# Performance work log

Measured on AMD Instinct MI355X. Metric: run time of the kernel, lower is better.

The kernel has to match this reference:

```python
import jax, jax.numpy as jnp
import numpy as np

DIM = 384
HD = 64
SCALE = float(HD ** 0.5)


def _linear_params(key, out_f, in_f):
    kw, kb = jax.random.split(key)
    bound = 1.0 / np.sqrt(in_f)
    W = jax.random.uniform(kw, (out_f, in_f), jnp.float32, -bound, bound)
    b = jax.random.uniform(kb, (out_f,), jnp.float32, -bound, bound)
    return W, b


def setup_inputs() -> dict:
    key = jax.random.key(0)
    ks = jax.random.split(key, 12)
    N = 8192
    situation = jax.random.normal(ks[0], (DIM,), jnp.float32)
    turn_embeddings = jax.random.normal(ks[1], (N, DIM), jnp.float32)
    bilinear_scores = jax.random.normal(ks[2], (N,), jnp.float32)
    Wt, bt = _linear_params(ks[3], HD, DIM + 1)      # turn_proj
    Ws, bs = _linear_params(ks[4], HD, DIM)          # situation_proj
    Wsaq, bsaq = _linear_params(ks[5], HD, HD)
    Wsak, bsak = _linear_params(ks[6], HD, HD)
    Wsav, bsav = _linear_params(ks[7], HD, HD)
    Wcq, bcq = _linear_params(ks[8], HD, HD)
    Wck, bck = _linear_params(ks[9], HD, HD)
    Wcv, bcv = _linear_params(ks[10], HD, HD)
    # score_head is zero-initialized in the module; use small random values so
    # the output is non-trivial for kernel correctness testing.
    Wsc, bsc = _linear_params(ks[11], 1, HD)
    residual_gate = jnp.float32(-5.0)
    return dict(situation=situation, turn_embeddings=turn_embeddings,
                bilinear_scores=bilinear_scores,
                Wt=Wt, bt=bt, Ws=Ws, bs=bs,
                Wsaq=Wsaq, bsaq=bsaq, Wsak=Wsak, bsak=bsak, Wsav=Wsav, bsav=bsav,
                Wcq=Wcq, bcq=bcq, Wck=Wck, bck=bck, Wcv=Wcv, bcv=bcv,
                Wsc=Wsc, bsc=bsc, residual_gate=residual_gate)


def reference(situation, turn_embeddings, bilinear_scores,
              Wt, bt, Ws, bs,
              Wsaq, bsaq, Wsak, bsak, Wsav, bsav,
              Wcq, bcq, Wck, bck, Wcv, bcv,
              Wsc, bsc, residual_gate):
    # [N, dim+1] = [turn_embedding; bilinear_score]
    turn_features = jnp.concatenate([turn_embeddings, bilinear_scores[:, None]], axis=-1)
    turn_hidden = turn_features @ Wt.T + bt                      # [N, HD]
    # self-attention among turns (dropout = identity, eval mode)
    sa_q = turn_hidden @ Wsaq.T + bsaq
    sa_k = turn_hidden @ Wsak.T + bsak
    sa_v = turn_hidden @ Wsav.T + bsav
    sa_weights = jax.nn.softmax((sa_q @ sa_k.T) / SCALE, axis=-1)  # [N, N]
    turn_hidden = turn_hidden + sa_weights @ sa_v
    # sigmoid cross-attention against the single situation vector
    sit_hidden = (situation @ Ws.T + bs)[None, :]                # [1, HD]
    ca_q = turn_hidden @ Wcq.T + bcq                             # [N, HD]
    ca_k = sit_hidden @ Wck.T + bck                              # [1, HD]
    ca_v = sit_hidden @ Wcv.T + bcv                              # [1, HD]
    ca_weights = jax.nn.sigmoid((ca_q @ ca_k.T) / SCALE)         # [N, 1]
    combined = turn_hidden + ca_weights * ca_v                   # [N, HD]
    attention_scores = (combined @ Wsc.T + bsc)[:, 0]            # [N]
    gate = jax.nn.sigmoid(residual_gate)
    return (1.0 - gate) * bilinear_scores + gate * attention_scores
```

## Files before the change

kernel.cpp:

```cpp
#include <hip/hip_runtime.h>
#include <hip/hip_bf16.h>

typedef __attribute__((ext_vector_type(8))) short short8;
typedef __attribute__((ext_vector_type(4))) float f32x4;
typedef __attribute__((ext_vector_type(2))) long long2t;

__device__ __forceinline__ short f2bf(float x) {
  union { float f; unsigned u; } a; a.f = x;
  unsigned r = (a.u + 0x7FFFu + ((a.u >> 16) & 1u)) >> 16;
  return (short)r;
}
__device__ __forceinline__ float bf2f(short x) {
  union { unsigned u; float f; } a; a.u = ((unsigned)(unsigned short)x) << 16;
  return a.f;
}
__device__ __forceinline__ unsigned cvtpk(float lo, float hi) {
  unsigned r;
  asm("v_cvt_pk_bf16_f32 %0, %1, %2" : "=v"(r) : "v"(lo), "v"(hi));
  return r;
}
__device__ __forceinline__ unsigned pk8(float a, float b, float c, float d) {
  unsigned lo, hi;
  asm("v_cvt_pk_fp8_f32 %0, %1, %2" : "=v"(lo) : "v"(a), "v"(b));
  asm("v_cvt_pk_fp8_f32 %0, %1, %2" : "=v"(hi) : "v"(c), "v"(d));
  return (lo & 0xffffu) | (hi << 16);
}
__device__ __forceinline__ long2t as_l2(uint4 v) {
  union { uint4 u; long2t l; } cc; cc.u = v; return cc.l;
}
__device__ __forceinline__ void gload16(const void* g, void* l) {
  __builtin_amdgcn_global_load_lds((const __attribute__((address_space(1))) unsigned int*)g,
                                   (__attribute__((address_space(3))) unsigned int*)l, 16, 0, 0);
}

__global__ __launch_bounds__(256) void ca_proj4(
    const float* __restrict__ te, const float* __restrict__ bil,
    const float* __restrict__ Wt, const float* __restrict__ bt,
    const float* __restrict__ Wsaq, const float* __restrict__ bq,
    const float* __restrict__ Wsak, const float* __restrict__ bk2,
    const float* __restrict__ Wsav, const float* __restrict__ bv,
    short* __restrict__ hb, unsigned char* __restrict__ qb8,
    unsigned char* __restrict__ kb8, unsigned char* __restrict__ vl8,
    const float* __restrict__ sit, const float* __restrict__ Ws, const float* __restrict__ bs,
    const float* __restrict__ Wck, const float* __restrict__ bck,
    const float* __restrict__ Wcv, const float* __restrict__ bcv,
    const float* __restrict__ Wcq, const float* __restrict__ bcq,
    const float* __restrict__ Wsc, float* __restrict__ u_ws, float* __restrict__ scal,
    int N) {
  __shared__ float Pp[8192];
  __shared__ short Hl[32][72];
  __shared__ unsigned char Q8[32][72];
  __shared__ unsigned char K8[32][72];
  __shared__ unsigned char V8s[64][32];
  __shared__ float part[4][64];
  __shared__ float sh[64], ck[64], cv[64];
  const int t = threadIdx.x;
  if ((int)blockIdx.x == (N >> 5)) {
    int j = t & 63, p = t >> 6;
    float a = 0.f;
    for (int d = p * 96; d < p * 96 + 96; ++d) a += Ws[j * 384 + d] * sit[d];
    part[p][j] = a;
    __syncthreads();
    if (t < 64) sh[t] = part[0][t] + part[1][t] + part[2][t] + part[3][t] + bs[t];
    __syncthreads();
    if (t < 64) {
      float kk = bck[t], vv = bcv[t];
      for (int d = 0; d < 64; ++d) { kk += Wck[t * 64 + d] * sh[d]; vv += Wcv[t * 64 + d] * sh[d]; }
      ck[t] = kk; cv[t] = vv;
    }
    __syncthreads();
    if (t < 64) {
      float uu = 0.f;
      for (int jj = 0; jj < 64; ++jj) uu += Wcq[jj * 64 + t] * ck[jj];
      u_ws[t] = uu;
    }
    if (t == 0) {
      float c0 = 0.f, cw = 0.f;
      for (int jj = 0; jj < 64; ++jj) { c0 += bcq[jj] * ck[jj]; cw += cv[jj] * Wsc[jj]; }
      scal[0] = c0; scal[1] = cw;
    }
    return;
  }
  const int lane = t & 63, w = t >> 6;
  const int g = lane >> 4, li = lane & 15;
  const int i0 = blockIdx.x * 32;

  f32x4 acc[2][4];
#pragma unroll
  for (int qs = 0; qs < 2; ++qs)
#pragma unroll
    for (int n = 0; n < 4; ++n) acc[qs][n] = (f32x4){0.f, 0.f, 0.f, 0.f};
  const int kw = w * 96;
#pragma unroll
  for (int ks = 0; ks < 3; ++ks) {
    short8 af[2];
#pragma unroll
    for (int qs = 0; qs < 2; ++qs) {
      const float* ap = te + (size_t)(i0 + qs * 16 + li) * 384 + kw + ks * 32 + g * 8;
      float4 a0 = *(const float4*)ap;
      float4 a1 = *(const float4*)(ap + 4);
      af[qs][0] = f2bf(a0.x); af[qs][1] = f2bf(a0.y); af[qs][2] = f2bf(a0.z); af[qs][3] = f2bf(a0.w);
      af[qs][4] = f2bf(a1.x); af[qs][5] = f2bf(a1.y); af[qs][6] = f2bf(a1.z); af[qs][7] = f2bf(a1.w);
    }
#pragma unroll
    for (int n = 0; n < 4; ++n) {
      short8 bf;
      const float* wp = Wt + (size_t)(n * 16 + li) * 385 + kw + ks * 32 + g * 8;
#pragma unroll
      for (int jj = 0; jj < 8; ++jj) bf[jj] = f2bf(wp[jj]);
      acc[0][n] = __builtin_amdgcn_mfma_f32_16x16x32_bf16(af[0], bf, acc[0][n], 0, 0, 0);
      acc[1][n] = __builtin_amdgcn_mfma_f32_16x16x32_bf16(af[1], bf, acc[1][n], 0, 0, 0);
    }
  }
#pragma unroll
  for (int qs = 0; qs < 2; ++qs)
#pragma unroll
    for (int n = 0; n < 4; ++n)
      *(f32x4*)&Pp[((w * 8 + qs * 4 + n) * 64 + lane) * 4] = acc[qs][n];
  __syncthreads();
#pragma unroll
  for (int ss = 0; ss < 2; ++ss) {
    int s = t + ss * 256;
    int qs2 = s >> 8, n2 = (s >> 6) & 3, lane2 = s & 63;
    int g2 = lane2 >> 4, li2 = lane2 & 15;
    int base = (qs2 * 4 + n2) * 256 + lane2 * 4;
    f32x4 v0 = *(const f32x4*)&Pp[base];
    f32x4 v1 = *(const f32x4*)&Pp[base + 2048];
    f32x4 v2 = *(const f32x4*)&Pp[base + 4096];
    f32x4 v3 = *(const f32x4*)&Pp[base + 6144];
    int col = n2 * 16 + li2;
    float wc = Wt[(size_t)col * 385 + 384], bb = bt[col];
#pragma unroll
    for (int r = 0; r < 4; ++r) {
      int row = qs2 * 16 + g2 * 4 + r;
      float val = v0[r] + v1[r] + v2[r] + v3[r] + bb + bil[i0 + row] * wc;
      Hl[row][col] = f2bf(val);
    }
  }
  __syncthreads();
  {
    int row = t >> 3, seg = t & 7;
    *(uint4*)&hb[(size_t)(i0 + row) * 64 + seg * 8] = *(uint4*)&Hl[row][seg * 8];
  }
  short8 ha[2][2];
#pragma unroll
  for (int qs = 0; qs < 2; ++qs)
#pragma unroll
    for (int ks = 0; ks < 2; ++ks)
      ha[qs][ks] = *(const short8*)&Hl[qs * 16 + li][ks * 32 + g * 8];
  const float* Wm[3] = {Wsaq, Wsak, Wsav};
  f32x4 pacc[3][2];
#pragma unroll
  for (int m = 0; m < 3; ++m)
#pragma unroll
    for (int qs = 0; qs < 2; ++qs) pacc[m][qs] = (f32x4){0.f, 0.f, 0.f, 0.f};
#pragma unroll
  for (int m = 0; m < 3; ++m)
#pragma unroll
    for (int ks = 0; ks < 2; ++ks) {
      const float* wp = Wm[m] + (size_t)(w * 16 + li) * 64 + ks * 32 + g * 8;
      float4 b0 = *(const float4*)wp;
      float4 b1 = *(const float4*)(wp + 4);
      short8 bf;
      bf[0] = f2bf(b0.x); bf[1] = f2bf(b0.y); bf[2] = f2bf(b0.z); bf[3] = f2bf(b0.w);
      bf[4] = f2bf(b1.x); bf[5] = f2bf(b1.y); bf[6] = f2bf(b1.z); bf[7] = f2bf(b1.w);
      pacc[m][0] = __builtin_amdgcn_mfma_f32_16x16x32_bf16(ha[0][ks], bf, pacc[m][0], 0, 0, 0);
      pacc[m][1] = __builtin_amdgcn_mfma_f32_16x16x32_bf16(ha[1][ks], bf, pacc[m][1], 0, 0, 0);
    }
  const int col = w * 16 + li;
  const float QSC = 0.18033688011112042f;
  {
    float bbq = bq[col], bbk = bk2[col], bbv = bv[col];
#pragma unroll
    for (int qs = 0; qs < 2; ++qs) {
      unsigned uq = pk8((pacc[0][qs][0] + bbq) * QSC, (pacc[0][qs][1] + bbq) * QSC,
                        (pacc[0][qs][2] + bbq) * QSC, (pacc[0][qs][3] + bbq) * QSC);
      unsigned uk = pk8(pacc[1][qs][0] + bbk, pacc[1][qs][1] + bbk,
                        pacc[1][qs][2] + bbk, pacc[1][qs][3] + bbk);
      unsigned uv = pk8(pacc[2][qs][0] + bbv, pacc[2][qs][1] + bbv,
                        pacc[2][qs][2] + bbv, pacc[2][qs][3] + bbv);
#pragma unroll
      for (int r = 0; r < 4; ++r) {
        Q8[qs * 16 + g * 4 + r][col] = (unsigned char)(uq >> (8 * r));
        K8[qs * 16 + g * 4 + r][col] = (unsigned char)(uk >> (8 * r));
      }
      *(unsigned*)&V8s[col][qs * 16 + g * 4] = uv;
    }
  }
  __syncthreads();
  {
    const int h = t & 1, l2 = (t >> 1) & 63, loc = t >> 7;
    const int srow = (l2 & 15) + 16 * loc;
    const int scol = h * 32 + (l2 >> 4) * 8;
    unsigned long vq = *(const unsigned long*)&Q8[srow][scol];
    *(unsigned long*)(qb8 + ((size_t)((i0 >> 4) + loc) * 1024 + l2 * 16 + h * 8)) = vq;
    unsigned long vk = *(const unsigned long*)&K8[srow][scol];
    *(unsigned long*)(kb8 + ((size_t)((i0 >> 6) * 4 + ((i0 >> 4) & 3) + loc) * 1024 + l2 * 16 + h * 8)) = vk;
    const int dt = t >> 6, l3 = t & 63;
    unsigned long vv = *(const unsigned long*)&V8s[dt * 16 + (l3 & 15)][(l3 >> 4) * 8];
    *(unsigned long*)(vl8 + ((size_t)((i0 >> 6) * 4 + dt) * 1024 + l3 * 16 + ((i0 >> 5) & 1) * 8)) = vv;
  }
}

__global__ __launch_bounds__(128, 2) void ca_attn7(
    const uint4* __restrict__ qb8, const unsigned* __restrict__ kb8,
    const unsigned* __restrict__ vl8,
    unsigned* __restrict__ pOu, float* __restrict__ pL, int N) {
  __shared__ unsigned Kl[2][1024];
  __shared__ unsigned Vl[2][1024];
  __shared__ unsigned Pl[2][2][256];
  const int t = threadIdx.x, lane = t & 63, wid = t >> 6;
  const int g = lane >> 4, li = lane & 15;
  const int bid = blockIdx.x;
  const int sp = bid & 7, qblk = bid >> 3;
  const int i0 = qblk * 64 + wid * 32;
  const int ntil = N >> 9;
  const int tile0 = sp * ntil;

#define STG(b, T)                                                                       \
  do {                                                                                  \
    gload16(kb8 + (((size_t)(T) * 4 + 2 * wid) << 8) + lane * 4,     &Kl[b][(2 * wid) * 256]);     \
    gload16(kb8 + (((size_t)(T) * 4 + 2 * wid + 1) << 8) + lane * 4, &Kl[b][(2 * wid + 1) * 256]); \
    gload16(vl8 + (((size_t)(T) * 4 + 2 * wid) << 8) + lane * 4,     &Vl[b][(2 * wid) * 256]);     \
    gload16(vl8 + (((size_t)(T) * 4 + 2 * wid + 1) << 8) + lane * 4, &Vl[b][(2 * wid + 1) * 256]); \
  } while (0)

  long2t qf[2];
  qf[0] = as_l2(qb8[(size_t)((i0 >> 4) + 0) * 64 + lane]);
  qf[1] = as_l2(qb8[(size_t)((i0 >> 4) + 1) * 64 + lane]);

  f32x4 acc[2][4];
  float rs[2] = {0.f, 0.f};
#pragma unroll
  for (int qs = 0; qs < 2; ++qs)
#pragma unroll
    for (int n = 0; n < 4; ++n) acc[qs][n] = (f32x4){0.f, 0.f, 0.f, 0.f};

  STG(0, tile0);
  asm volatile("s_waitcnt vmcnt(0)" ::: "memory");

  for (int tt = 0; tt < ntil; ++tt) {
    const int cur = tt & 1;
    __builtin_amdgcn_s_barrier();
    if (tt + 1 < ntil) STG(cur ^ 1, tile0 + tt + 1);

    f32x4 s4[2][4];
#pragma unroll
    for (int qs = 0; qs < 2; ++qs)
#pragma unroll
      for (int t4 = 0; t4 < 4; ++t4) s4[qs][t4] = (f32x4){0.f, 0.f, 0.f, 0.f};
    __builtin_amdgcn_s_setprio(1);
#pragma unroll
    for (int t4 = 0; t4 < 4; ++t4) {
      long2t kl = as_l2(*(const uint4*)&Kl[cur][t4 * 256 + lane * 4]);
      s4[0][t4] = __builtin_amdgcn_mfma_f32_16x16x32_fp8_fp8(kl.x, qf[0].x, s4[0][t4], 0, 0, 0);
      s4[0][t4] = __builtin_amdgcn_mfma_f32_16x16x32_fp8_fp8(kl.y, qf[0].y, s4[0][t4], 0, 0, 0);
      s4[1][t4] = __builtin_amdgcn_mfma_f32_16x16x32_fp8_fp8(kl.x, qf[1].x, s4[1][t4], 0, 0, 0);
      s4[1][t4] = __builtin_amdgcn_mfma_f32_16x16x32_fp8_fp8(kl.y, qf[1].y, s4[1][t4], 0, 0, 0);
    }
    __builtin_amdgcn_s_setprio(0);
#pragma unroll
    for (int qs = 0; qs < 2; ++qs) {
#pragma unroll
      for (int t4 = 0; t4 < 4; ++t4) {
        float p0, p1, p2, p3;
        asm("v_exp_f32 %0, %1" : "=v"(p0) : "v"(s4[qs][t4][0]));
        asm("v_exp_f32 %0, %1" : "=v"(p1) : "v"(s4[qs][t4][1]));
        asm("v_exp_f32 %0, %1" : "=v"(p2) : "v"(s4[qs][t4][2]));
        asm("v_exp_f32 %0, %1" : "=v"(p3) : "v"(s4[qs][t4][3]));
        rs[qs] += (p0 + p1) + (p2 + p3);
        unsigned u = pk8(p0, p1, p2, p3);
        Pl[wid][qs][(li + 16 * ((t4 & 1) * 2 + (g >> 1))) * 4 + (t4 >> 1) * 2 + (g & 1)] = u;
      }
    }
    asm volatile("s_waitcnt lgkmcnt(0)" ::: "memory");
#pragma unroll
    for (int qs = 0; qs < 2; ++qs) {
      long2t pf = as_l2(*(const uint4*)&Pl[wid][qs][lane * 4]);
      __builtin_amdgcn_s_setprio(1);
#pragma unroll
      for (int dt = 0; dt < 4; ++dt) {
        long2t vf = as_l2(*(const uint4*)&Vl[cur][dt * 256 + lane * 4]);
        acc[qs][dt] = __builtin_amdgcn_mfma_f32_16x16x32_fp8_fp8(pf.x, vf.x, acc[qs][dt], 0, 0, 0);
        acc[qs][dt] = __builtin_amdgcn_mfma_f32_16x16x32_fp8_fp8(pf.y, vf.y, acc[qs][dt], 0, 0, 0);
      }
      __builtin_amdgcn_s_setprio(0);
    }
    asm volatile("s_waitcnt vmcnt(0)" ::: "memory");
  }
#undef STG

  const size_t ob = ((size_t)sp * (N >> 5) + (i0 >> 5)) * 2;
#pragma unroll
  for (int qs = 0; qs < 2; ++qs) {
#pragma unroll
    for (int dt = 0; dt < 4; ++dt) {
      uint2 wv;
      wv.x = cvtpk(acc[qs][dt][0], acc[qs][dt][1]);
      wv.y = cvtpk(acc[qs][dt][2], acc[qs][dt][3]);
      *(uint2*)&pOu[((ob + qs) * 4 + dt) * 128 + lane * 2] = wv;
    }
    float r2 = rs[qs] + __shfl_xor(rs[qs], 16, 64);
    r2 += __shfl_xor(r2, 32, 64);
    if (lane < 16) pL[(size_t)sp * N + i0 + qs * 16 + lane] = r2;
  }
}

__global__ __launch_bounds__(256) void ca_merge3(
    const short* __restrict__ hb, const unsigned* __restrict__ pOu, const float* __restrict__ pL,
    const float* __restrict__ u_ws, const float* __restrict__ scal,
    const float* __restrict__ bil, const float* __restrict__ Wsc,
    const float* __restrict__ bsc_p, const float* __restrict__ rgate_p,
    float* __restrict__ out, int N) {
  const int t = threadIdx.x;
  const int rp = t >> 3, e = t & 7;
  const int dt2 = e >> 1, li0 = (e & 1) * 8;
  const float gate = 1.f / (1.f + __expf(-rgate_p[0]));
  const float bsc = bsc_p[0], sc0 = scal[0], sc1 = scal[1];
  const int R0 = blockIdx.x * 64 + rp * 2;
  const int b32 = R0 >> 5, qs2 = (R0 >> 4) & 1, g2 = (R0 >> 2) & 3;
  const int rpair = (R0 & 3) >> 1;
  float o0[8], o1[8], L0 = 0.f, L1 = 0.f;
#pragma unroll
  for (int j = 0; j < 8; ++j) { o0[j] = 0.f; o1[j] = 0.f; }
#pragma unroll
  for (int sp2 = 0; sp2 < 8; ++sp2) {
    size_t base = ((((size_t)sp2 * (N >> 5) + b32) * 2 + qs2) * 4 + dt2) * 128
                  + (g2 * 16 + li0) * 2 + rpair;
#pragma unroll
    for (int j = 0; j < 8; ++j) {
      unsigned u = pOu[base + 2 * j];
      o0[j] += bf2f((short)(u & 0xffff));
      o1[j] += bf2f((short)(u >> 16));
    }
    L0 += pL[(size_t)sp2 * N + R0];
    L1 += pL[(size_t)sp2 * N + R0 + 1];
  }
  const float iL0 = 1.f / L0, iL1 = 1.f / L1;
  const int c0 = dt2 * 16 + li0;
  short8 hv0 = *(const short8*)&hb[(size_t)R0 * 64 + c0];
  short8 hv1 = *(const short8*)&hb[(size_t)(R0 + 1) * 64 + c0];
  float s1a = 0.f, s2a = 0.f, s1b = 0.f, s2b = 0.f;
#pragma unroll
  for (int j = 0; j < 8; ++j) {
    float uwsj = u_ws[c0 + j], wscj = Wsc[c0 + j];
    float h0 = bf2f(hv0[j]) + o0[j] * iL0;
    float h1 = bf2f(hv1[j]) + o1[j] * iL1;
    s1a += h0 * uwsj; s2a += h0 * wscj;
    s1b += h1 * uwsj; s2b += h1 * wscj;
  }
#pragma unroll
  for (int mask = 1; mask < 8; mask <<= 1) {
    s1a += __shfl_xor(s1a, mask, 64);
    s2a += __shfl_xor(s2a, mask, 64);
    s1b += __shfl_xor(s1b, mask, 64);
    s2b += __shfl_xor(s2b, mask, 64);
  }
  if (e == 0) {
    float cawa = 1.f / (1.f + __expf(-(s1a + sc0) * 0.125f));
    float cawb = 1.f / (1.f + __expf(-(s1b + sc0) * 0.125f));
    float scoreA = s2a + cawa * sc1 + bsc;
    float scoreB = s2b + cawb * sc1 + bsc;
    out[R0] = (1.f - gate) * bil[R0] + gate * scoreA;
    out[R0 + 1] = (1.f - gate) * bil[R0 + 1] + gate * scoreB;
  }
}

extern "C" void kernel_launch(void* const* d_in, const int* in_sizes, int n_in,
                              void* d_out, int out_size, void* d_ws, size_t ws_size,
                              hipStream_t stream) {
  const float* sit  = (const float*)d_in[0];
  const float* te   = (const float*)d_in[1];
  const float* bil  = (const float*)d_in[2];
  const float* Wt   = (const float*)d_in[3];
  const float* bt   = (const float*)d_in[4];
  const float* Ws   = (const float*)d_in[5];
  const float* bs   = (const float*)d_in[6];
  const float* Wsaq = (const float*)d_in[7];
  const float* bsaq = (const float*)d_in[8];
  const float* Wsak = (const float*)d_in[9];
  const float* bsak = (const float*)d_in[10];
  const float* Wsav = (const float*)d_in[11];
  const float* bsav = (const float*)d_in[12];
  const float* Wcq  = (const float*)d_in[13];
  const float* bcq  = (const float*)d_in[14];
  const float* Wck  = (const float*)d_in[15];
  const float* bck  = (const float*)d_in[16];
  const float* Wcv  = (const float*)d_in[17];
  const float* bcv  = (const float*)d_in[18];
  const float* Wsc  = (const float*)d_in[19];
  const float* bsc  = (const float*)d_in[20];
  const float* rgate= (const float*)d_in[21];
  const int N = in_sizes[2];

  char* w = (char*)d_ws;
  size_t off = 0;
  short* hbuf        = (short*)(w + off);         off += (size_t)N * 64 * 2;
  unsigned char* qb8 = (unsigned char*)(w + off); off += (size_t)N * 64;
  unsigned char* kb8 = (unsigned char*)(w + off); off += (size_t)N * 64;
  unsigned char* vl8 = (unsigned char*)(w + off); off += (size_t)N * 64;
  float* u_ws        = (float*)(w + off);         off += 64 * 4;
  float* scal        = (float*)(w + off);         off += 4 * 4;
  unsigned* pOu      = (unsigned*)(w + off);      off += (size_t)8 * N * 64 * 2;
  float* pL          = (float*)(w + off);         off += (size_t)8 * N * 4;

  ca_proj4<<<N / 32 + 1, 256, 0, stream>>>(te, bil, Wt, bt, Wsaq, bsaq, Wsak, bsak,
                                           Wsav, bsav, hbuf, qb8, kb8, vl8,
                                           sit, Ws, bs, Wck, bck, Wcv, bcv, Wcq, bcq, Wsc,
                                           u_ws, scal, N);
  ca_attn7<<<N / 8, 128, 0, stream>>>((const uint4*)qb8, (const unsigned*)kb8,
                                      (const unsigned*)vl8, pOu, pL, N);
  ca_merge3<<<N / 64, 256, 0, stream>>>(hbuf, pOu, pL, u_ws, scal, bil, Wsc, bsc, rgate,
                                        (float*)d_out, N);
}
```

Measured before the change: 50.61 us.

## Fold Q/K/V projections into turn projection via precombined weight matrix

Adds a small pre-kernel that multiplies the Q/K/V weights into the turn projection weights (and folds the bilinear column and biases), producing a 256x384 bf16 combined matrix. The projection kernel then does one K=384 GEMM per wave yielding H, Q, K and V directly, removing the cross-wave split-K reduction through shared memory, the second chained GEMM and several block barriers. It also reorders the PV MFMA loop in the attention kernel to share V fragment loads across both query subtiles. This costs an extra kernel launch and four times the MFMA work on the 384-wide input, and it changes rounding because Q/K/V no longer pass through bf16-rounded H.

New measurement: 61.69 us. +21.9%, slower.

```diff
diff --git a/kernel.cpp b/kernel.cpp
--- a/kernel.cpp
+++ b/kernel.cpp
@@ -33,29 +33,50 @@
                                    (__attribute__((address_space(3))) unsigned int*)l, 16, 0, 0);
 }
 
-__global__ __launch_bounds__(256) void ca_proj4(
-    const float* __restrict__ te, const float* __restrict__ bil,
+#define QSC 0.18033688011112042f
+
+__global__ __launch_bounds__(256) void ca_comb(
     const float* __restrict__ Wt, const float* __restrict__ bt,
-    const float* __restrict__ Wsaq, const float* __restrict__ bq,
-    const float* __restrict__ Wsak, const float* __restrict__ bk2,
-    const float* __restrict__ Wsav, const float* __restrict__ bv,
-    short* __restrict__ hb, unsigned char* __restrict__ qb8,
-    unsigned char* __restrict__ kb8, unsigned char* __restrict__ vl8,
+    const float* __restrict__ Wsaq, const float* __restrict__ bsaq,
+    const float* __restrict__ Wsak, const float* __restrict__ bsak,
+    const float* __restrict__ Wsav, const float* __restrict__ bsav,
+    short* __restrict__ Wcomb, float* __restrict__ wcol4, float* __restrict__ bias4,
     const float* __restrict__ sit, const float* __restrict__ Ws, const float* __restrict__ bs,
     const float* __restrict__ Wck, const float* __restrict__ bck,
     const float* __restrict__ Wcv, const float* __restrict__ bcv,
     const float* __restrict__ Wcq, const float* __restrict__ bcq,
-    const float* __restrict__ Wsc, float* __restrict__ u_ws, float* __restrict__ scal,
-    int N) {
-  __shared__ float Pp[8192];
-  __shared__ short Hl[32][72];
-  __shared__ unsigned char Q8[32][72];
-  __shared__ unsigned char K8[32][72];
-  __shared__ unsigned char V8s[64][32];
+    const float* __restrict__ Wsc, float* __restrict__ u_ws, float* __restrict__ scal) {
+  const int bid = blockIdx.x, t = threadIdx.x;
+  if (bid < 96) {
+    __shared__ float Wtc[64][4];
+    const int c0 = bid * 4;
+    { int j = t & 63, cc = t >> 6; Wtc[j][cc] = Wt[(size_t)j * 385 + c0 + cc]; }
+    __syncthreads();
+    const int r = t;
+    float o[4] = {0.f, 0.f, 0.f, 0.f};
+    if (r < 64) {
+#pragma unroll
+      for (int cc = 0; cc < 4; ++cc) o[cc] = Wtc[r][cc];
+    } else {
+      const int m = (r >> 6) - 1, rr = r & 63;
+      const float* Wm = (m == 0 ? Wsaq : m == 1 ? Wsak : Wsav) + (size_t)rr * 64;
+      for (int j = 0; j < 64; ++j) {
+        float wv = Wm[j];
+#pragma unroll
+        for (int cc = 0; cc < 4; ++cc) o[cc] += wv * Wtc[j][cc];
+      }
+      if (m == 0) {
+#pragma unroll
+        for (int cc = 0; cc < 4; ++cc) o[cc] *= QSC;
+      }
+    }
+#pragma unroll
+    for (int cc = 0; cc < 4; ++cc) Wcomb[(size_t)r * 384 + c0 + cc] = f2bf(o[cc]);
+    return;
+  }
   __shared__ float part[4][64];
   __shared__ float sh[64], ck[64], cv[64];
-  const int t = threadIdx.x;
-  if ((int)blockIdx.x == (N >> 5)) {
+  {
     int j = t & 63, p = t >> 6;
     float a = 0.f;
     for (int d = p * 96; d < p * 96 + 96; ++d) a += Ws[j * 384 + d] * sit[d];
@@ -75,13 +96,47 @@
       u_ws[t] = uu;
     }
     if (t == 0) {
-      float c0 = 0.f, cw = 0.f;
-      for (int jj = 0; jj < 64; ++jj) { c0 += bcq[jj] * ck[jj]; cw += cv[jj] * Wsc[jj]; }
-      scal[0] = c0; scal[1] = cw;
-    }
-    return;
-  }
-  const int lane = t & 63, w = t >> 6;
+      float c0s = 0.f, cw = 0.f;
+      for (int jj = 0; jj < 64; ++jj) { c0s += bcq[jj] * ck[jj]; cw += cv[jj] * Wsc[jj]; }
+      scal[0] = c0s; scal[1] = cw;
+    }
+  }
+  {
+    const int r = t;
+    float wc, bb;
+    if (r < 64) {
+      wc = Wt[(size_t)r * 385 + 384];
+      bb = bt[r];
+    } else {
+      const int m = (r >> 6) - 1, rr = r & 63;
+      const float* Wm = (m == 0 ? Wsaq : m == 1 ? Wsak : Wsav) + (size_t)rr * 64;
+      const float* bm = (m == 0 ? bsaq : m == 1 ? bsak : bsav);
+      float s1 = 0.f, s2 = 0.f;
+      for (int j = 0; j < 64; ++j) {
+        float wv = Wm[j];
+        s1 += wv * Wt[(size_t)j * 385 + 384];
+        s2 += wv * bt[j];
+      }
+      float sc = (m == 0) ? QSC : 1.f;
+      wc = sc * s1;
+      bb = sc * (s2 + bm[rr]);
+    }
+    wcol4[r] = wc;
+    bias4[r] = bb;
+  }
+}
+
+__global__ __launch_bounds__(256) void ca_proj5(
+    const float* __restrict__ te, const float* __restrict__ bil,
+    const short* __restrict__ Wcomb, const float* __restrict__ wcol4,
+    const float* __restrict__ bias4,
+    short* __restrict__ hb, unsigned char* __restrict__ qb8,
+    unsigned char* __restrict__ kb8, unsigned char* __restrict__ vl8, int N) {
+  __shared__ short Hl[32][72];
+  __shared__ unsigned char Q8[32][72];
+  __shared__ unsigned char K8[32][72];
+  __shared__ unsigned char V8s[64][32];
+  const int t = threadIdx.x, lane = t & 63, w = t >> 6;
   const int g = lane >> 4, li = lane & 15;
   const int i0 = blockIdx.x * 32;
 
@@ -90,13 +145,13 @@
   for (int qs = 0; qs < 2; ++qs)
 #pragma unroll
     for (int n = 0; n < 4; ++n) acc[qs][n] = (f32x4){0.f, 0.f, 0.f, 0.f};
-  const int kw = w * 96;
-#pragma unroll
-  for (int ks = 0; ks < 3; ++ks) {
+
+#pragma unroll 4
+  for (int ks = 0; ks < 12; ++ks) {
     short8 af[2];
 #pragma unroll
     for (int qs = 0; qs < 2; ++qs) {
-      const float* ap = te + (size_t)(i0 + qs * 16 + li) * 384 + kw + ks * 32 + g * 8;
+      const float* ap = te + (size_t)(i0 + qs * 16 + li) * 384 + ks * 32 + g * 8;
       float4 a0 = *(const float4*)ap;
       float4 a1 = *(const float4*)(ap + 4);
       af[qs][0] = f2bf(a0.x); af[qs][1] = f2bf(a0.y); af[qs][2] = f2bf(a0.z); af[qs][3] = f2bf(a0.w);
@@ -104,101 +159,104 @@
     }
 #pragma unroll
     for (int n = 0; n < 4; ++n) {
-      short8 bf;
-      const float* wp = Wt + (size_t)(n * 16 + li) * 385 + kw + ks * 32 + g * 8;
-#pragma unroll
-      for (int jj = 0; jj < 8; ++jj) bf[jj] = f2bf(wp[jj]);
+      short8 bf = *(const short8*)&Wcomb[(size_t)(w * 64 + n * 16 + li) * 384 + ks * 32 + g * 8];
       acc[0][n] = __builtin_amdgcn_mfma_f32_16x16x32_bf16(af[0], bf, acc[0][n], 0, 0, 0);
       acc[1][n] = __builtin_amdgcn_mfma_f32_16x16x32_bf16(af[1], bf, acc[1][n], 0, 0, 0);
     }
   }
+
+  float bilv[2][4];
 #pragma unroll
   for (int qs = 0; qs < 2; ++qs)
 #pragma unroll
-    for (int n = 0; n < 4; ++n)
-      *(f32x4*)&Pp[((w * 8 + qs * 4 + n) * 64 + lane) * 4] = acc[qs][n];
-  __syncthreads();
-#pragma unroll
-  for (int ss = 0; ss < 2; ++ss) {
-    int s = t + ss * 256;
-    int qs2 = s >> 8, n2 = (s >> 6) & 3, lane2 = s & 63;
-    int g2 = lane2 >> 4, li2 = lane2 & 15;
-    int base = (qs2 * 4 + n2) * 256 + lane2 * 4;
-    f32x4 v0 = *(const f32x4*)&Pp[base];
-    f32x4 v1 = *(const f32x4*)&Pp[base + 2048];
-    f32x4 v2 = *(const f32x4*)&Pp[base + 4096];
-    f32x4 v3 = *(const f32x4*)&Pp[base + 6144];
-    int col = n2 * 16 + li2;
-    float wc = Wt[(size_t)col * 385 + 384], bb = bt[col];
-#pragma unroll
-    for (int r = 0; r < 4; ++r) {
-      int row = qs2 * 16 + g2 * 4 + r;
-      float val = v0[r] + v1[r] + v2[r] + v3[r] + bb + bil[i0 + row] * wc;
-      Hl[row][col] = f2bf(val);
-    }
-  }
-  __syncthreads();
-  {
-    int row = t >> 3, seg = t & 7;
-    *(uint4*)&hb[(size_t)(i0 + row) * 64 + seg * 8] = *(uint4*)&Hl[row][seg * 8];
-  }
-  short8 ha[2][2];
-#pragma unroll
-  for (int qs = 0; qs < 2; ++qs)
-#pragma unroll
-    for (int ks = 0; ks < 2; ++ks)
-      ha[qs][ks] = *(const short8*)&Hl[qs * 16 + li][ks * 32 + g * 8];
-  const float* Wm[3] = {Wsaq, Wsak, Wsav};
-  f32x4 pacc[3][2];
-#pragma unroll
-  for (int m = 0; m < 3; ++m)
-#pragma unroll
-    for (int qs = 0; qs < 2; ++qs) pacc[m][qs] = (f32x4){0.f, 0.f, 0.f, 0.f};
-#pragma unroll
-  for (int m = 0; m < 3; ++m)
-#pragma unroll
-    for (int ks = 0; ks < 2; ++ks) {
-      const float* wp = Wm[m] + (size_t)(w * 16 + li) * 64 + ks * 32 + g * 8;
-      float4 b0 = *(const float4*)wp;
-      float4 b1 = *(const float4*)(wp + 4);
-      short8 bf;
-      bf[0] = f2bf(b0.x); bf[1] = f2bf(b0.y); bf[2] = f2bf(b0.z); bf[3] = f2bf(b0.w);
-      bf[4] = f2bf(b1.x); bf[5] = f2bf(b1.y); bf[6] = f2bf(b1.z); bf[7] = f2bf(b1.w);
-      pacc[m][0] = __builtin_amdgcn_mfma_f32_16x16x32_bf16(ha[0][ks], bf, pacc[m][0], 0, 0, 0);
-      pacc[m][1] = __builtin_amdgcn_mfma_f32_16x16x32_bf16(ha[1][ks], bf, pacc[m][1], 0, 0, 0);
-    }
-  const int col = w * 16 + li;
-  const float QSC = 0.18033688011112042f;
-  {
-    float bbq = bq[col], bbk = bk2[col], bbv = bv[col];
+    for (int r = 0; r < 4; ++r) bilv[qs][r] = bil[i0 + qs * 16 + g * 4 + r];
+  float bb[4], wc[4];
+#pragma unroll
+  for (int n = 0; n < 4; ++n) {
+    bb[n] = bias4[w * 64 + n * 16 + li];
+    wc[n] = wcol4[w * 64 + n * 16 + li];
+  }
+
+  if (w == 0) {
+#pragma unroll
+    for (int qs = 0; qs < 2; ++qs)
+#pragma unroll
+      for (int n = 0; n < 4; ++n)
+#pragma unroll
+        for (int r = 0; r < 4; ++r)
+          Hl[qs * 16 + g * 4 + r][n * 16 + li] =
+              f2bf(acc[qs][n][r] + bb[n] + bilv[qs][r] * wc[n]);
+    asm volatile("s_waitcnt lgkmcnt(0)" ::: "memory");
+    __builtin_amdgcn_sched_barrier(0);
+    const int row = lane >> 1, sb = (lane & 1) * 4;
+#pragma unroll
+    for (int k = 0; k < 4; ++k)
+      *(uint4*)&hb[(size_t)(i0 + row) * 64 + (sb + k) * 8] = *(const uint4*)&Hl[row][(sb + k) * 8];
+  } else if (w == 1) {
+#pragma unroll
+    for (int qs = 0; qs < 2; ++qs)
+#pragma unroll
+      for (int n = 0; n < 4; ++n) {
+        unsigned u = pk8(acc[qs][n][0] + bb[n] + bilv[qs][0] * wc[n],
+                         acc[qs][n][1] + bb[n] + bilv[qs][1] * wc[n],
+                         acc[qs][n][2] + bb[n] + bilv[qs][2] * wc[n],
+                         acc[qs][n][3] + bb[n] + bilv[qs][3] * wc[n]);
+#pragma unroll
+        for (int r = 0; r < 4; ++r)
+          Q8[qs * 16 + g * 4 + r][n * 16 + li] = (unsigned char)(u >> (8 * r));
+      }
+    asm volatile("s_waitcnt lgkmcnt(0)" ::: "memory");
+    __builtin_amdgcn_sched_barrier(0);
 #pragma unroll
     for (int qs = 0; qs < 2; ++qs) {
-      unsigned uq = pk8((pacc[0][qs][0] + bbq) * QSC, (pacc[0][qs][1] + bbq) * QSC,
-                        (pacc[0][qs][2] + bbq) * QSC, (pacc[0][qs][3] + bbq) * QSC);
-      unsigned uk = pk8(pacc[1][qs][0] + bbk, pacc[1][qs][1] + bbk,
-                        pacc[1][qs][2] + bbk, pacc[1][qs][3] + bbk);
-      unsigned uv = pk8(pacc[2][qs][0] + bbv, pacc[2][qs][1] + bbv,
-                        pacc[2][qs][2] + bbv, pacc[2][qs][3] + bbv);
-#pragma unroll
-      for (int r = 0; r < 4; ++r) {
-        Q8[qs * 16 + g * 4 + r][col] = (unsigned char)(uq >> (8 * r));
-        K8[qs * 16 + g * 4 + r][col] = (unsigned char)(uk >> (8 * r));
-      }
-      *(unsigned*)&V8s[col][qs * 16 + g * 4] = uv;
-    }
-  }
-  __syncthreads();
-  {
-    const int h = t & 1, l2 = (t >> 1) & 63, loc = t >> 7;
-    const int srow = (l2 & 15) + 16 * loc;
-    const int scol = h * 32 + (l2 >> 4) * 8;
-    unsigned long vq = *(const unsigned long*)&Q8[srow][scol];
-    *(unsigned long*)(qb8 + ((size_t)((i0 >> 4) + loc) * 1024 + l2 * 16 + h * 8)) = vq;
-    unsigned long vk = *(const unsigned long*)&K8[srow][scol];
-    *(unsigned long*)(kb8 + ((size_t)((i0 >> 6) * 4 + ((i0 >> 4) & 3) + loc) * 1024 + l2 * 16 + h * 8)) = vk;
-    const int dt = t >> 6, l3 = t & 63;
-    unsigned long vv = *(const unsigned long*)&V8s[dt * 16 + (l3 & 15)][(l3 >> 4) * 8];
-    *(unsigned long*)(vl8 + ((size_t)((i0 >> 6) * 4 + dt) * 1024 + l3 * 16 + ((i0 >> 5) & 1) * 8)) = vv;
+      unsigned long long lo = *(const unsigned long long*)&Q8[qs * 16 + li][g * 8];
+      unsigned long long hi = *(const unsigned long long*)&Q8[qs * 16 + li][32 + g * 8];
+      unsigned char* dst = qb8 + (size_t)((i0 >> 4) + qs) * 1024 + lane * 16;
+      *(unsigned long long*)dst = lo;
+      *(unsigned long long*)(dst + 8) = hi;
+    }
+  } else if (w == 2) {
+#pragma unroll
+    for (int qs = 0; qs < 2; ++qs)
+#pragma unroll
+      for (int n = 0; n < 4; ++n) {
+        unsigned u = pk8(acc[qs][n][0] + bb[n] + bilv[qs][0] * wc[n],
+                         acc[qs][n][1] + bb[n] + bilv[qs][1] * wc[n],
+                         acc[qs][n][2] + bb[n] + bilv[qs][2] * wc[n],
+                         acc[qs][n][3] + bb[n] + bilv[qs][3] * wc[n]);
+#pragma unroll
+        for (int r = 0; r < 4; ++r)
+          K8[qs * 16 + g * 4 + r][n * 16 + li] = (unsigned char)(u >> (8 * r));
+      }
+    asm volatile("s_waitcnt lgkmcnt(0)" ::: "memory");
+    __builtin_amdgcn_sched_barrier(0);
+#pragma unroll
+    for (int qs = 0; qs < 2; ++qs) {
+      unsigned long long lo = *(const unsigned long long*)&K8[qs * 16 + li][g * 8];
+      unsigned long long hi = *(const unsigned long long*)&K8[qs * 16 + li][32 + g * 8];
+      unsigned char* dst = kb8 + (size_t)((i0 >> 6) * 4 + ((i0 >> 4) & 3) + qs) * 1024 + lane * 16;
+      *(unsigned long long*)dst = lo;
+      *(unsigned long long*)(dst + 8) = hi;
+    }
+  } else {
+#pragma unroll
+    for (int qs = 0; qs < 2; ++qs)
+#pragma unroll
+      for (int n = 0; n < 4; ++n) {
+        unsigned u = pk8(acc[qs][n][0] + bb[n] + bilv[qs][0] * wc[n],
+                         acc[qs][n][1] + bb[n] + bilv[qs][1] * wc[n],
+                         acc[qs][n][2] + bb[n] + bilv[qs][2] * wc[n],
+                         acc[qs][n][3] + bb[n] + bilv[qs][3] * wc[n]);
+        *(unsigned*)&V8s[n * 16 + li][qs * 16 + g * 4] = u;
+      }
+    asm volatile("s_waitcnt lgkmcnt(0)" ::: "memory");
+    __builtin_amdgcn_sched_barrier(0);
+#pragma unroll
+    for (int dt = 0; dt < 4; ++dt) {
+      unsigned long long v = *(const unsigned long long*)&V8s[dt * 16 + li][g * 8];
+      *(unsigned long long*)(vl8 + (size_t)((i0 >> 6) * 4 + dt) * 1024 + lane * 16 +
+                             ((i0 >> 5) & 1) * 8) = v;
+    }
   }
 }
 
@@ -217,8 +275,8 @@
   const int ntil = N >> 9;
   const int tile0 = sp * ntil;
 
-#define STG(b, T)                                                                       \
-  do {                                                                                  \
+#define STG(b, T)                                                                                  \
+  do {                                                                                             \
     gload16(kb8 + (((size_t)(T) * 4 + 2 * wid) << 8) + lane * 4,     &Kl[b][(2 * wid) * 256]);     \
     gload16(kb8 + (((size_t)(T) * 4 + 2 * wid + 1) << 8) + lane * 4, &Kl[b][(2 * wid + 1) * 256]); \
     gload16(vl8 + (((size_t)(T) * 4 + 2 * wid) << 8) + lane * 4,     &Vl[b][(2 * wid) * 256]);     \
@@ -274,18 +332,18 @@
       }
     }
     asm volatile("s_waitcnt lgkmcnt(0)" ::: "memory");
-#pragma unroll
-    for (int qs = 0; qs < 2; ++qs) {
-      long2t pf = as_l2(*(const uint4*)&Pl[wid][qs][lane * 4]);
-      __builtin_amdgcn_s_setprio(1);
-#pragma unroll
-      for (int dt = 0; dt < 4; ++dt) {
-        long2t vf = as_l2(*(const uint4*)&Vl[cur][dt * 256 + lane * 4]);
-        acc[qs][dt] = __builtin_amdgcn_mfma_f32_16x16x32_fp8_fp8(pf.x, vf.x, acc[qs][dt], 0, 0, 0);
-        acc[qs][dt] = __builtin_amdgcn_mfma_f32_16x16x32_fp8_fp8(pf.y, vf.y, acc[qs][dt], 0, 0, 0);
-      }
-      __builtin_amdgcn_s_setprio(0);
-    }
+    long2t pf0 = as_l2(*(const uint4*)&Pl[wid][0][lane * 4]);
+    long2t pf1 = as_l2(*(const uint4*)&Pl[wid][1][lane * 4]);
+    __builtin_amdgcn_s_setprio(1);
+#pragma unroll
+    for (int dt = 0; dt < 4; ++dt) {
+      long2t vf = as_l2(*(const uint4*)&Vl[cur][dt * 256 + lane * 4]);
+      acc[0][dt] = __builtin_amdgcn_mfma_f32_16x16x32_fp8_fp8(pf0.x, vf.x, acc[0][dt], 0, 0, 0);
+      acc[0][dt] = __builtin_amdgcn_mfma_f32_16x16x32_fp8_fp8(pf0.y, vf.y, acc[0][dt], 0, 0, 0);
+      acc[1][dt] = __builtin_amdgcn_mfma_f32_16x16x32_fp8_fp8(pf1.x, vf.x, acc[1][dt], 0, 0, 0);
+      acc[1][dt] = __builtin_amdgcn_mfma_f32_16x16x32_fp8_fp8(pf1.y, vf.y, acc[1][dt], 0, 0, 0);
+    }
+    __builtin_amdgcn_s_setprio(0);
     asm volatile("s_waitcnt vmcnt(0)" ::: "memory");
   }
 #undef STG
@@ -401,13 +459,17 @@
   unsigned char* vl8 = (unsigned char*)(w + off); off += (size_t)N * 64;
   float* u_ws        = (float*)(w + off);         off += 64 * 4;
   float* scal        = (float*)(w + off);         off += 4 * 4;
+  short* Wcomb       = (short*)(w + off);         off += (size_t)256 * 384 * 2;
+  float* wcol4       = (float*)(w + off);         off += 256 * 4;
+  float* bias4       = (float*)(w + off);         off += 256 * 4;
   unsigned* pOu      = (unsigned*)(w + off);      off += (size_t)8 * N * 64 * 2;
   float* pL          = (float*)(w + off);         off += (size_t)8 * N * 4;
 
-  ca_proj4<<<N / 32 + 1, 256, 0, stream>>>(te, bil, Wt, bt, Wsaq, bsaq, Wsak, bsak,
-                                           Wsav, bsav, hbuf, qb8, kb8, vl8,
-                                           sit, Ws, bs, Wck, bck, Wcv, bcv, Wcq, bcq, Wsc,
-                                           u_ws, scal, N);
+  ca_comb<<<97, 256, 0, stream>>>(Wt, bt, Wsaq, bsaq, Wsak, bsak, Wsav, bsav,
+                                  Wcomb, wcol4, bias4,
+                                  sit, Ws, bs, Wck, bck, Wcv, bcv, Wcq, bcq, Wsc, u_ws, scal);
+  ca_proj5<<<N / 32, 256, 0, stream>>>(te, bil, Wcomb, wcol4, bias4,
+                                       hbuf, qb8, kb8, vl8, N);
   ca_attn7<<<N / 8, 128, 0, stream>>>((const uint4*)qb8, (const unsigned*)kb8,
                                       (const unsigned*)vl8, pOu, pL, N);
   ca_merge3<<<N / 64, 256, 0, stream>>>(hbuf, pOu, pL, u_ws, scal, bil, Wsc, bsc, rgate,
```
